# Optimization experiments

Measured on AMD Instinct MI355X. Metric: run time of the kernel, lower is better.

Reference implementation:

```python
import jax, jax.numpy as jnp
import numpy as np

B, T, V, E, H, O = 64, 2048, 50000, 256, 256, 16

def setup_inputs() -> dict:
    key = jax.random.key(0)
    ks = jax.random.split(key, 10)
    s_rnn = 1.0 / np.sqrt(H)
    s_fc1 = 1.0 / np.sqrt(H)
    s_fc2 = 1.0 / np.sqrt(H // 2)
    return {
        "x": jax.random.randint(ks[0], (B, T), 0, V, dtype=jnp.int32),
        "emb": jax.random.normal(ks[1], (V, E), dtype=jnp.float32),
        "W_ih": jax.random.uniform(ks[2], (H, E), jnp.float32, -s_rnn, s_rnn),
        "W_hh": jax.random.uniform(ks[3], (H, H), jnp.float32, -s_rnn, s_rnn),
        "b_ih": jax.random.uniform(ks[4], (H,), jnp.float32, -s_rnn, s_rnn),
        "b_hh": jax.random.uniform(ks[5], (H,), jnp.float32, -s_rnn, s_rnn),
        "fc1_w": jax.random.uniform(ks[6], (H // 2, H), jnp.float32, -s_fc1, s_fc1),
        "fc1_b": jax.random.uniform(ks[7], (H // 2,), jnp.float32, -s_fc1, s_fc1),
        "fc2_w": jax.random.uniform(ks[8], (O, H // 2), jnp.float32, -s_fc2, s_fc2),
        "fc2_b": jax.random.uniform(ks[9], (O,), jnp.float32, -s_fc2, s_fc2),
    }

def reference(x, emb, W_ih, W_hh, b_ih, b_hh, fc1_w, fc1_b, fc2_w, fc2_b):
    # Embedding lookup: [B, T, E]
    e = emb[x]
    # Precompute input-to-hidden projection for all timesteps in one big GEMM
    xh = jnp.einsum("bte,he->bth", e, W_ih) + b_ih + b_hh  # [B, T, H]
    h0 = jnp.zeros((x.shape[0], W_hh.shape[0]), dtype=e.dtype)

    def step(h, xt):  # h: [B, H], xt: [B, H]
        h = jnp.tanh(xt + h @ W_hh.T)
        return h, None

    h_last, _ = jax.lax.scan(step, h0, jnp.swapaxes(xh, 0, 1))  # final hidden [B, H]
    # Dropout is identity at inference. MLP head: fc1 -> relu -> fc2
    hid = jax.nn.relu(h_last @ fc1_w.T + fc1_b)
    return hid @ fc2_w.T + fc2_b  # [B, O]
```

## Files before the change

kernel.cpp:

```cpp
#include <hip/hip_runtime.h>
#include <hip/hip_bf16.h>


#define B_  64
#define T_  2048
#define E_  256
#define H_  256
#define O_  16
#define H2_ 128
#define CH  4
#define HP  272

typedef _Float16 f16x2 __attribute__((ext_vector_type(2)));
typedef _Float16 f16x4 __attribute__((ext_vector_type(4)));
typedef _Float16 f16x8 __attribute__((ext_vector_type(8)));
typedef float    f32x4 __attribute__((ext_vector_type(4)));

#define LDS_BARRIER() asm volatile("s_waitcnt lgkmcnt(0)\n\ts_barrier" ::: "memory")

__device__ __forceinline__ float tanh_fast(float x) {
  const float e = __expf(2.0f * x);
  return fmaf(-2.0f, __builtin_amdgcn_rcpf(e + 1.0f), 1.0f);
}

__device__ __forceinline__ f32x4 cvt4(f16x4 v) {
  return (f32x4){(float)v[0], (float)v[1], (float)v[2], (float)v[3]};
}

__global__ __launch_bounds__(256) void k0_cvt(
    const float* __restrict__ W_ih, const float* __restrict__ W_hh,
    _Float16* __restrict__ Wih16, _Float16* __restrict__ Whh16) {
  const int i = (blockIdx.x * 256 + threadIdx.x) * 4;
  if (i < H_ * E_) {
    float4 a = *(const float4*)&W_ih[i];
    float4 b = *(const float4*)&W_hh[i];
    f16x4 ah, bh;
    ah[0]=(_Float16)a.x; ah[1]=(_Float16)a.y; ah[2]=(_Float16)a.z; ah[3]=(_Float16)a.w;
    bh[0]=(_Float16)b.x; bh[1]=(_Float16)b.y; bh[2]=(_Float16)b.z; bh[3]=(_Float16)b.w;
    *(f16x4*)&Wih16[i] = ah;
    *(f16x4*)&Whh16[i] = bh;
  }
}

__global__ __launch_bounds__(256) void k1_xh(
    const int* __restrict__ x, const float* __restrict__ emb,
    const _Float16* __restrict__ Wih16, const float* __restrict__ b_ih,
    const float* __restrict__ b_hh, _Float16* __restrict__ xh) {
  __shared__ _Float16 A16[64][264];
  const int tid  = threadIdx.x;
  const int w    = tid >> 6;
  const int lane = tid & 63;
  const int nl   = lane & 15;
  const int koff = (lane >> 4) << 3;
  const long r0  = (long)blockIdx.x * 64;

  {
    const int c4 = lane << 2;
#pragma unroll
    for (int it = 0; it < 16; ++it) {
      const int row = (it << 2) + w;
      const long tok = x[r0 + row];
      const float4 v = *(const float4*)&emb[tok * E_ + c4];
      f16x4 hv;
      hv[0] = (_Float16)v.x; hv[1] = (_Float16)v.y;
      hv[2] = (_Float16)v.z; hv[3] = (_Float16)v.w;
      *(f16x4*)&A16[row][c4] = hv;
    }
  }

  f16x8 bfr[4][8];
#pragma unroll
  for (int nt = 0; nt < 4; ++nt) {
    const int n = (w << 6) + (nt << 4) + nl;
#pragma unroll
    for (int kt = 0; kt < 8; ++kt)
      bfr[nt][kt] = *(const f16x8*)&Wih16[n * E_ + (kt << 5) + koff];
  }
  __syncthreads();

  f32x4 acc[4][4];
#pragma unroll
  for (int mt = 0; mt < 4; ++mt)
#pragma unroll
    for (int nt = 0; nt < 4; ++nt) acc[mt][nt] = (f32x4){};

#pragma unroll
  for (int mt = 0; mt < 4; ++mt) {
#pragma unroll
    for (int kt = 0; kt < 8; ++kt) {
      const f16x8 a = *(const f16x8*)&A16[(mt << 4) + nl][(kt << 5) + koff];
#pragma unroll
      for (int nt = 0; nt < 4; ++nt)
        acc[mt][nt] = __builtin_amdgcn_mfma_f32_16x16x32_f16(a, bfr[nt][kt], acc[mt][nt], 0, 0, 0);
    }
  }
  __syncthreads();

  {
    const int rsub = (lane >> 4) << 2;
#pragma unroll
    for (int nt = 0; nt < 4; ++nt) {
      const int n = (w << 6) + (nt << 4) + nl;
      const float bias = b_ih[n] + b_hh[n];
#pragma unroll
      for (int mt = 0; mt < 4; ++mt)
#pragma unroll
        for (int j = 0; j < 4; ++j)
          A16[(mt << 4) + rsub + j][n] = (_Float16)(acc[mt][nt][j] + bias);
    }
  }
  __syncthreads();

  {
#pragma unroll
    for (int i = 0; i < 8; ++i) {
      const int row = (w << 4) + (i << 1) + (lane >> 5);
      const int col = (lane & 31) << 3;
      *(f16x8*)&xh[(r0 + row) * H_ + col] = *(const f16x8*)&A16[row][col];
    }
  }
}

__global__ __attribute__((amdgpu_flat_work_group_size(512, 512)))
__attribute__((amdgpu_waves_per_eu(2, 2))) void k2_rnn(
    const _Float16* __restrict__ xh, const _Float16* __restrict__ Whh16,
    const float* __restrict__ fc1_w, const float* __restrict__ fc1_b,
    const float* __restrict__ fc2_w, const float* __restrict__ fc2_b,
    float* __restrict__ out) {
  __shared__ _Float16 whh_s[H_ * H_];
  __shared__ _Float16 h16[2][CH][HP];
  __shared__ float    hid_s[CH][H2_ + 4];

  const int tid   = threadIdx.x;
  const int w     = tid >> 6;
  const int lane  = tid & 63;
  const int nl    = lane & 15;
  const int quad  = lane >> 4;
  const int cc    = nl & (CH - 1);
  const int g     = nl >> 2;
  const int mtsel = g & 1;
  const int jp    = g >> 1;
  const int koff  = quad << 3;
  const int rwb   = (w << 5) + (quad << 2);
  const int c0    = blockIdx.x * CH;

  {
#pragma unroll
    for (int c = 0; c < 16; ++c) {
      const int idx = ((c << 9) + tid) << 3;
      *(f16x8*)&whh_s[idx] = *(const f16x8*)&Whh16[idx];
    }
  }
  if (tid < 128) *(f16x8*)&h16[0][tid >> 5][(tid & 31) << 3] = (f16x8){};
  __syncthreads();

  f16x8 afr[2][8];
#pragma unroll
  for (int mt = 0; mt < 2; ++mt) {
    const int r = (w << 5) + (mt << 4) + nl;
#pragma unroll
    for (int kt = 0; kt < 8; ++kt)
      afr[mt][kt] = *(const f16x8*)&whh_s[r * H_ + (kt << 5) + koff];
  }

  const _Float16* xb = xh + (size_t)(c0 + cc) * T_ * H_ + rwb;
  f16x4 xq0[4], xq1[4], xn0[4], xn1[4];
#pragma unroll
  for (int s = 0; s < 4; ++s) {
    xq0[s] = *(const f16x4*)&xb[(size_t)s * H_];
    xq1[s] = *(const f16x4*)&xb[(size_t)s * H_ + 16];
  }
#pragma unroll
  for (int s = 0; s < 4; ++s) {
    xn0[s] = *(const f16x4*)&xb[(size_t)(4 + s) * H_];
    xn1[s] = *(const f16x4*)&xb[(size_t)(4 + s) * H_ + 16];
  }

#define BODY(P, S)                                                             \
  {                                                                            \
    f16x8 bfr[8];                                                              \
    _Pragma("unroll")                                                          \
    for (int i = 0; i < 8; ++i)                                                \
      bfr[i] = *(const f16x8*)&h16[P][cc][(i << 5) + koff];                    \
    f32x4 ca0 = __builtin_amdgcn_mfma_f32_16x16x32_f16(afr[0][0], bfr[0], cvt4(xq0[S]), 0, 0, 0); \
    f32x4 ca1 = __builtin_amdgcn_mfma_f32_16x16x32_f16(afr[1][0], bfr[0], cvt4(xq1[S]), 0, 0, 0); \
    f32x4 cb0 = __builtin_amdgcn_mfma_f32_16x16x32_f16(afr[0][4], bfr[4], (f32x4){}, 0, 0, 0); \
    f32x4 cb1 = __builtin_amdgcn_mfma_f32_16x16x32_f16(afr[1][4], bfr[4], (f32x4){}, 0, 0, 0); \
    _Pragma("unroll")                                                          \
    for (int i = 1; i < 4; ++i) {                                              \
      ca0 = __builtin_amdgcn_mfma_f32_16x16x32_f16(afr[0][i], bfr[i], ca0, 0, 0, 0);         \
      ca1 = __builtin_amdgcn_mfma_f32_16x16x32_f16(afr[1][i], bfr[i], ca1, 0, 0, 0);         \
      cb0 = __builtin_amdgcn_mfma_f32_16x16x32_f16(afr[0][4 + i], bfr[4 + i], cb0, 0, 0, 0); \
      cb1 = __builtin_amdgcn_mfma_f32_16x16x32_f16(afr[1][4 + i], bfr[4 + i], cb1, 0, 0, 0); \
    }                                                                          \
    const f32x4 s0 = ca0 + cb0;                                                \
    const f32x4 s1 = ca1 + cb1;                                                \
    const f32x4 sm = mtsel ? s1 : s0;                                          \
    const float u0 = jp ? sm[2] : sm[0];                                       \
    const float u1 = jp ? sm[3] : sm[1];                                       \
    f16x2 o;                                                                   \
    o[0] = (_Float16)tanh_fast(u0);                                            \
    o[1] = (_Float16)tanh_fast(u1);                                            \
    *(f16x2*)&h16[P ^ 1][cc][rwb + (mtsel << 4) + (jp << 1)] = o;              \
    LDS_BARRIER();                                                             \
  }

  for (int tt = 0; tt < T_; tt += 4) {
    BODY(0, 0)
    BODY(1, 1)
    BODY(0, 2)
    BODY(1, 3)
#pragma unroll
    for (int s = 0; s < 4; ++s) { xq0[s] = xn0[s]; xq1[s] = xn1[s]; }
    const int tn = tt + 8;
#pragma unroll
    for (int s = 0; s < 4; ++s) {
      const size_t ti = (size_t)((tn + s) & (T_ - 1)) * H_;
      xn0[s] = *(const f16x4*)&xb[ti];
      xn1[s] = *(const f16x4*)&xb[ti + 16];
    }
  }
#undef BODY

  __syncthreads();

  {
    const int pc = tid >> 7;
    const int o_ = tid & 127;
    float s = fc1_b[o_];
#pragma unroll 8
    for (int k = 0; k < H_; ++k) s += fc1_w[o_ * H_ + k] * (float)h16[0][pc][k];
    hid_s[pc][o_] = fmaxf(s, 0.f);
  }
  __syncthreads();
  if (tid < CH * O_) {
    const int c = tid >> 4, o_ = tid & 15;
    float s = fc2_b[o_];
#pragma unroll 8
    for (int k = 0; k < H2_; ++k) s += fc2_w[o_ * H2_ + k] * hid_s[c][k];
    out[(size_t)(c0 + c) * O_ + o_] = s;
  }
}

extern "C" void kernel_launch(void* const* d_in, const int* in_sizes, int n_in,
                              void* d_out, int out_size, void* d_ws, size_t ws_size,
                              hipStream_t stream) {
  const int*   x     = (const int*)d_in[0];
  const float* emb   = (const float*)d_in[1];
  const float* W_ih  = (const float*)d_in[2];
  const float* W_hh  = (const float*)d_in[3];
  const float* b_ih  = (const float*)d_in[4];
  const float* b_hh  = (const float*)d_in[5];
  const float* fc1_w = (const float*)d_in[6];
  const float* fc1_b = (const float*)d_in[7];
  const float* fc2_w = (const float*)d_in[8];
  const float* fc2_b = (const float*)d_in[9];
  float* outp = (float*)d_out;

  _Float16* xh16  = (_Float16*)d_ws;
  _Float16* Wih16 = xh16 + (size_t)B_ * T_ * H_;
  _Float16* Whh16 = Wih16 + (size_t)H_ * E_;

  k0_cvt<<<dim3(H_ * E_ / 1024), dim3(256), 0, stream>>>(W_ih, W_hh, Wih16, Whh16);
  k1_xh<<<dim3(B_ * T_ / 64), dim3(256), 0, stream>>>(x, emb, Wih16, b_ih, b_hh, xh16);
  k2_rnn<<<dim3(B_ / CH), dim3(512), 0, stream>>>(xh16, Whh16, fc1_w, fc1_b, fc2_w, fc2_b, outp);
}
```

Before: 1.312 ms.

## Fuse xh projection and RNN scan into one producer/consumer kernel with flags

```diff
diff --git a/kernel.cpp b/kernel.cpp
--- a/kernel.cpp
+++ b/kernel.cpp
@@ -10,6 +10,9 @@
 #define H2_ 128
 #define CH  4
 #define HP  272
+#define NCONS 16
+#define NPROD 1024
+#define SMEM_BYTES 137536
 
 typedef _Float16 f16x2 __attribute__((ext_vector_type(2)));
 typedef _Float16 f16x4 __attribute__((ext_vector_type(4)));
@@ -28,110 +31,124 @@
 }
 
 __global__ __launch_bounds__(256) void k0_cvt(
-    const float* __restrict__ W_ih, const float* __restrict__ W_hh,
-    _Float16* __restrict__ Wih16, _Float16* __restrict__ Whh16) {
+    const float* __restrict__ W_ih, _Float16* __restrict__ Wih16,
+    int* __restrict__ flags) {
   const int i = (blockIdx.x * 256 + threadIdx.x) * 4;
   if (i < H_ * E_) {
     float4 a = *(const float4*)&W_ih[i];
-    float4 b = *(const float4*)&W_hh[i];
-    f16x4 ah, bh;
+    f16x4 ah;
     ah[0]=(_Float16)a.x; ah[1]=(_Float16)a.y; ah[2]=(_Float16)a.z; ah[3]=(_Float16)a.w;
-    bh[0]=(_Float16)b.x; bh[1]=(_Float16)b.y; bh[2]=(_Float16)b.z; bh[3]=(_Float16)b.w;
     *(f16x4*)&Wih16[i] = ah;
-    *(f16x4*)&Whh16[i] = bh;
-  }
-}
-
-__global__ __launch_bounds__(256) void k1_xh(
+  }
+  if (blockIdx.x == 0) {
+#pragma unroll
+    for (int j = 0; j < 8; ++j) flags[(threadIdx.x << 3) + j] = 0;
+  }
+}
+
+__global__ __attribute__((amdgpu_flat_work_group_size(512, 512)))
+__attribute__((amdgpu_waves_per_eu(2, 2))) void k1k2(
     const int* __restrict__ x, const float* __restrict__ emb,
     const _Float16* __restrict__ Wih16, const float* __restrict__ b_ih,
-    const float* __restrict__ b_hh, _Float16* __restrict__ xh) {
-  __shared__ _Float16 A16[64][264];
-  const int tid  = threadIdx.x;
-  const int w    = tid >> 6;
-  const int lane = tid & 63;
-  const int nl   = lane & 15;
-  const int koff = (lane >> 4) << 3;
-  const long r0  = (long)blockIdx.x * 64;
-
-  {
-    const int c4 = lane << 2;
-#pragma unroll
-    for (int it = 0; it < 16; ++it) {
-      const int row = (it << 2) + w;
-      const long tok = x[r0 + row];
-      const float4 v = *(const float4*)&emb[tok * E_ + c4];
-      f16x4 hv;
-      hv[0] = (_Float16)v.x; hv[1] = (_Float16)v.y;
-      hv[2] = (_Float16)v.z; hv[3] = (_Float16)v.w;
-      *(f16x4*)&A16[row][c4] = hv;
-    }
-  }
-
-  f16x8 bfr[4][8];
-#pragma unroll
-  for (int nt = 0; nt < 4; ++nt) {
-    const int n = (w << 6) + (nt << 4) + nl;
-#pragma unroll
-    for (int kt = 0; kt < 8; ++kt)
-      bfr[nt][kt] = *(const f16x8*)&Wih16[n * E_ + (kt << 5) + koff];
-  }
-  __syncthreads();
-
-  f32x4 acc[4][4];
-#pragma unroll
-  for (int mt = 0; mt < 4; ++mt)
-#pragma unroll
-    for (int nt = 0; nt < 4; ++nt) acc[mt][nt] = (f32x4){};
-
-#pragma unroll
-  for (int mt = 0; mt < 4; ++mt) {
-#pragma unroll
-    for (int kt = 0; kt < 8; ++kt) {
-      const f16x8 a = *(const f16x8*)&A16[(mt << 4) + nl][(kt << 5) + koff];
-#pragma unroll
-      for (int nt = 0; nt < 4; ++nt)
-        acc[mt][nt] = __builtin_amdgcn_mfma_f32_16x16x32_f16(a, bfr[nt][kt], acc[mt][nt], 0, 0, 0);
-    }
-  }
-  __syncthreads();
-
-  {
-    const int rsub = (lane >> 4) << 2;
-#pragma unroll
-    for (int nt = 0; nt < 4; ++nt) {
-      const int n = (w << 6) + (nt << 4) + nl;
-      const float bias = b_ih[n] + b_hh[n];
-#pragma unroll
-      for (int mt = 0; mt < 4; ++mt)
-#pragma unroll
-        for (int j = 0; j < 4; ++j)
-          A16[(mt << 4) + rsub + j][n] = (_Float16)(acc[mt][nt][j] + bias);
-    }
-  }
-  __syncthreads();
-
-  {
-#pragma unroll
-    for (int i = 0; i < 8; ++i) {
-      const int row = (w << 4) + (i << 1) + (lane >> 5);
-      const int col = (lane & 31) << 3;
-      *(f16x8*)&xh[(r0 + row) * H_ + col] = *(const f16x8*)&A16[row][col];
-    }
-  }
-}
-
-__global__ __attribute__((amdgpu_flat_work_group_size(512, 512)))
-__attribute__((amdgpu_waves_per_eu(2, 2))) void k2_rnn(
-    const _Float16* __restrict__ xh, const _Float16* __restrict__ Whh16,
+    const float* __restrict__ b_hh, _Float16* xh, int* flags,
+    const float* __restrict__ W_hh,
     const float* __restrict__ fc1_w, const float* __restrict__ fc1_b,
     const float* __restrict__ fc2_w, const float* __restrict__ fc2_b,
     float* __restrict__ out) {
-  __shared__ _Float16 whh_s[H_ * H_];
-  __shared__ _Float16 h16[2][CH][HP];
-  __shared__ float    hid_s[CH][H2_ + 4];
-
-  const int tid   = threadIdx.x;
+  __shared__ __align__(16) char smem[SMEM_BYTES];
+  const int tid = threadIdx.x;
+
+  if (blockIdx.x >= NCONS) {
+    const int pb   = blockIdx.x - NCONS;
+    const int seg2 = pb >> 6;
+    const int b    = pb & 63;
+    const int q    = tid >> 8;
+    const int stid = tid & 255;
+    const int w    = stid >> 6;
+    const int lane = stid & 63;
+    const int nl   = lane & 15;
+    const int koff = (lane >> 4) << 3;
+    const long r0  = (long)b * T_ + (long)((seg2 << 1) + q) * 64;
+    _Float16 (*A16)[264] = (_Float16(*)[264])(smem + (size_t)q * 33792);
+
+    {
+      const int c4 = lane << 2;
+#pragma unroll
+      for (int it = 0; it < 16; ++it) {
+        const int row = (it << 2) + w;
+        const long tok = x[r0 + row];
+        const float4 v = *(const float4*)&emb[tok * E_ + c4];
+        f16x4 hv;
+        hv[0] = (_Float16)v.x; hv[1] = (_Float16)v.y;
+        hv[2] = (_Float16)v.z; hv[3] = (_Float16)v.w;
+        *(f16x4*)&A16[row][c4] = hv;
+      }
+    }
+
+    f16x8 bfr[4][8];
+#pragma unroll
+    for (int nt = 0; nt < 4; ++nt) {
+      const int n = (w << 6) + (nt << 4) + nl;
+#pragma unroll
+      for (int kt = 0; kt < 8; ++kt)
+        bfr[nt][kt] = *(const f16x8*)&Wih16[n * E_ + (kt << 5) + koff];
+    }
+    __syncthreads();
+
+    f32x4 acc[4][4];
+#pragma unroll
+    for (int mt = 0; mt < 4; ++mt)
+#pragma unroll
+      for (int nt = 0; nt < 4; ++nt) acc[mt][nt] = (f32x4){};
+
+#pragma unroll
+    for (int mt = 0; mt < 4; ++mt) {
+#pragma unroll
+      for (int kt = 0; kt < 8; ++kt) {
+        const f16x8 a = *(const f16x8*)&A16[(mt << 4) + nl][(kt << 5) + koff];
+#pragma unroll
+        for (int nt = 0; nt < 4; ++nt)
+          acc[mt][nt] = __builtin_amdgcn_mfma_f32_16x16x32_f16(a, bfr[nt][kt], acc[mt][nt], 0, 0, 0);
+      }
+    }
+    __syncthreads();
+
+    {
+      const int rsub = (lane >> 4) << 2;
+#pragma unroll
+      for (int nt = 0; nt < 4; ++nt) {
+        const int n = (w << 6) + (nt << 4) + nl;
+        const float bias = b_ih[n] + b_hh[n];
+#pragma unroll
+        for (int mt = 0; mt < 4; ++mt)
+#pragma unroll
+          for (int j = 0; j < 4; ++j)
+            A16[(mt << 4) + rsub + j][n] = (_Float16)(acc[mt][nt][j] + bias);
+      }
+    }
+    __syncthreads();
+
+    {
+#pragma unroll
+      for (int i = 0; i < 8; ++i) {
+        const int row = (w << 4) + (i << 1) + (lane >> 5);
+        const int col = (lane & 31) << 3;
+        *(f16x8*)&xh[(r0 + row) * H_ + col] = *(const f16x8*)&A16[row][col];
+      }
+    }
+
+    __syncthreads();
+    if (stid == 0) {
+      const int fi = (b << 5) + (seg2 << 1) + q;
+      __hip_atomic_store(&flags[fi], 1, __ATOMIC_RELEASE, __HIP_MEMORY_SCOPE_AGENT);
+    }
+    return;
+  }
+
+  _Float16* whh_s = (_Float16*)smem;
+  _Float16 (*h16)[CH][HP] = (_Float16(*)[CH][HP])(smem + 131072);
+  float (*hid_s)[H2_ + 4] = (float(*)[H2_ + 4])(smem + 135424);
+
   const int w     = tid >> 6;
   const int lane  = tid & 63;
   const int nl    = lane & 15;
@@ -146,9 +163,13 @@
 
   {
 #pragma unroll
-    for (int c = 0; c < 16; ++c) {
-      const int idx = ((c << 9) + tid) << 3;
-      *(f16x8*)&whh_s[idx] = *(const f16x8*)&Whh16[idx];
+    for (int c = 0; c < 32; ++c) {
+      const int idx = ((c << 9) + tid) << 2;
+      const float4 v = *(const float4*)&W_hh[idx];
+      f16x4 hv;
+      hv[0] = (_Float16)v.x; hv[1] = (_Float16)v.y;
+      hv[2] = (_Float16)v.z; hv[3] = (_Float16)v.w;
+      *(f16x4*)&whh_s[idx] = hv;
     }
   }
   if (tid < 128) *(f16x8*)&h16[0][tid >> 5][(tid & 31) << 3] = (f16x8){};
@@ -162,6 +183,22 @@
     for (int kt = 0; kt < 8; ++kt)
       afr[mt][kt] = *(const f16x8*)&whh_s[r * H_ + (kt << 5) + koff];
   }
+
+#define WAIT_SEG(SEG)                                                          \
+  {                                                                            \
+    int _s = (SEG); if (_s > 31) _s = 31;                                      \
+    for (int c = 0; c < CH; ++c) {                                             \
+      const int fi = ((c0 + c) << 5) + _s;                                     \
+      int _tries = 0;                                                          \
+      while (__hip_atomic_load(&flags[fi], __ATOMIC_ACQUIRE,                   \
+                               __HIP_MEMORY_SCOPE_AGENT) == 0) {               \
+        __builtin_amdgcn_s_sleep(8);                                           \
+        if (++_tries > (1 << 21)) break;                                       \
+      }                                                                        \
+    }                                                                          \
+  }
+
+  WAIT_SEG(0);
 
   const _Float16* xb = xh + (size_t)(c0 + cc) * T_ * H_ + rwb;
   f16x4 xq0[4], xq1[4], xn0[4], xn1[4];
@@ -205,22 +242,26 @@
     LDS_BARRIER();                                                             \
   }
 
-  for (int tt = 0; tt < T_; tt += 4) {
-    BODY(0, 0)
-    BODY(1, 1)
-    BODY(0, 2)
-    BODY(1, 3)
-#pragma unroll
-    for (int s = 0; s < 4; ++s) { xq0[s] = xn0[s]; xq1[s] = xn1[s]; }
-    const int tn = tt + 8;
-#pragma unroll
-    for (int s = 0; s < 4; ++s) {
-      const size_t ti = (size_t)((tn + s) & (T_ - 1)) * H_;
-      xn0[s] = *(const f16x4*)&xb[ti];
-      xn1[s] = *(const f16x4*)&xb[ti + 16];
+  for (int ttc = 0; ttc < T_; ttc += 64) {
+    WAIT_SEG((ttc >> 6) + 1);
+    for (int tt = ttc; tt < ttc + 64; tt += 4) {
+      BODY(0, 0)
+      BODY(1, 1)
+      BODY(0, 2)
+      BODY(1, 3)
+#pragma unroll
+      for (int s = 0; s < 4; ++s) { xq0[s] = xn0[s]; xq1[s] = xn1[s]; }
+      const int tn = tt + 8;
+#pragma unroll
+      for (int s = 0; s < 4; ++s) {
+        const size_t ti = (size_t)((tn + s) & (T_ - 1)) * H_;
+        xn0[s] = *(const f16x4*)&xb[ti];
+        xn1[s] = *(const f16x4*)&xb[ti + 16];
+      }
     }
   }
 #undef BODY
+#undef WAIT_SEG
 
   __syncthreads();
 
@@ -259,9 +300,10 @@
 
   _Float16* xh16  = (_Float16*)d_ws;
   _Float16* Wih16 = xh16 + (size_t)B_ * T_ * H_;
-  _Float16* Whh16 = Wih16 + (size_t)H_ * E_;
-
-  k0_cvt<<<dim3(H_ * E_ / 1024), dim3(256), 0, stream>>>(W_ih, W_hh, Wih16, Whh16);
-  k1_xh<<<dim3(B_ * T_ / 64), dim3(256), 0, stream>>>(x, emb, Wih16, b_ih, b_hh, xh16);
-  k2_rnn<<<dim3(B_ / CH), dim3(512), 0, stream>>>(xh16, Whh16, fc1_w, fc1_b, fc2_w, fc2_b, outp);
-}
+  int*      flags = (int*)(Wih16 + (size_t)H_ * E_);
+
+  k0_cvt<<<dim3(H_ * E_ / 1024), dim3(256), 0, stream>>>(W_ih, Wih16, flags);
+  k1k2<<<dim3(NCONS + NPROD), dim3(512), 0, stream>>>(
+      x, emb, Wih16, b_ih, b_hh, xh16, flags, W_hh,
+      fc1_w, fc1_b, fc2_w, fc2_b, outp);
+}
```

Result: slower. 1.433 ms (+9.2%).
